# Kernel optimization log

Hardware: AMD Instinct MI355X
Metric: run time of the kernel (lower is better)

## Reference

```python
import jax, jax.numpy as jnp
import numpy as np

N_ENTITIES = 500000
N_RELATIONS = 16
DIM = 64
N_HOP = 2
BATCH = 256
N_MEMORY = 32


def setup_inputs() -> dict:
    key = jax.random.key(0)
    k1, k2, k3, k4, k5, k6 = jax.random.split(key, 6)
    entity_emb = jax.random.normal(k1, (N_ENTITIES + 1, DIM), dtype=jnp.float32) * 0.02
    relation_emb = jax.random.normal(k2, (N_RELATIONS, DIM), dtype=jnp.float32) * 0.02
    items = jax.random.randint(k3, (BATCH,), 0, N_ENTITIES)
    shape = (N_HOP, BATCH, N_RELATIONS, N_MEMORY)
    memories_h = jax.random.randint(k4, shape, 0, N_ENTITIES)
    memories_r = jax.random.randint(k5, shape, 0, N_RELATIONS)
    memories_t = jax.random.randint(k6, shape, 0, N_ENTITIES)
    return {
        "entity_emb": entity_emb,
        "relation_emb": relation_emb,
        "items": items,
        "memories_h": memories_h,
        "memories_r": memories_r,
        "memories_t": memories_t,
    }


def reference(entity_emb, relation_emb, items, memories_h, memories_r, memories_t):
    # items_emb / v: [B, D]
    v = entity_emb[items]

    def per_hop(mh, mr, mt):
        # gathers: [B, R, M, D]
        h = entity_emb[mh]
        r = relation_emb[mr]
        t = entity_emb[mt]
        # relation-modulated head: Rh = r * h  -> [B, R, M, D]
        Rh = r * h
        # attention scores against item embedding v: [B, R, M]
        scores = jnp.einsum("brmd,bd->brm", Rh, v)
        probs = jax.nn.softmax(scores, axis=-1)
        # weighted sum of tail embeddings: [B, R, D]
        return jnp.einsum("brmd,brm->brd", t, probs)

    # vmap over hop axis -> o: [n_hop, B, R, D]
    o = jax.vmap(per_hop)(memories_h, memories_r, memories_t)
    return o
```

## Files before the change

kernel.cpp:

```cpp
#include <hip/hip_runtime.h>
#include <hip/hip_bf16.h>

constexpr int BATCH = 256;
constexpr int NREL  = 16;
constexpr int DIM   = 64;
constexpr int NHOP  = 2;
constexpr int NMEM  = 32;

__global__ __launch_bounds__(256)
void kgan_kernel(const float* __restrict__ ent,
                 const float* __restrict__ rel,
                 const int*   __restrict__ items,
                 const int*   __restrict__ mh,
                 const int*   __restrict__ mr,
                 const int*   __restrict__ mt,
                 float*       __restrict__ out)
{
    __shared__ float rel_lds[NREL * DIM];
    {
        const int t = threadIdx.x;
        reinterpret_cast<float4*>(rel_lds)[t] =
            reinterpret_cast<const float4*>(rel)[t];
    }
    __syncthreads();

    const int gtid = blockIdx.x * blockDim.x + threadIdx.x;
    const int wave = gtid >> 6;
    const int lane = threadIdx.x & 63;
    const int sub  = lane >> 4;
    const int q    = lane & 15;

    const int b = (wave >> 4) & (BATCH - 1);

    const int item = items[b];
    const float4 v4 = reinterpret_cast<const float4*>(ent)[(size_t)item * 16 + q];

    const int base = wave * NMEM;
    const int lm   = lane & 31;
    const int vh   = mh[base + lm];
    const int vr   = mr[base + lm];
    const int vt   = mt[base + lm];

    const float4* ent4 = reinterpret_cast<const float4*>(ent);
    const float4* rl4  = reinterpret_cast<const float4*>(rel_lds);

    float4 hb[8], tb[8];
    int ridx[8];
    #pragma unroll
    for (int j = 0; j < 8; ++j) {
        const int hid = __shfl(vh, 4 * j + sub, 64);
        hb[j] = ent4[(size_t)hid * 16 + q];
    }
    #pragma unroll
    for (int j = 0; j < 8; ++j) {
        const int tid = __shfl(vt, 4 * j + sub, 64);
        tb[j] = ent4[(size_t)tid * 16 + q];
    }
    #pragma unroll
    for (int j = 0; j < 8; ++j)
        ridx[j] = __shfl(vr, 4 * j + sub, 64);

    float sc[8];
    #pragma unroll
    for (int j = 0; j < 8; ++j) {
        const float4 r4 = rl4[ridx[j] * 16 + q];
        const float4 h4 = hb[j];
        float p = h4.x * r4.x * v4.x;
        p = fmaf(h4.y * r4.y, v4.y, p);
        p = fmaf(h4.z * r4.z, v4.z, p);
        p = fmaf(h4.w * r4.w, v4.w, p);
        #pragma unroll
        for (int off = 8; off >= 1; off >>= 1)
            p += __shfl_xor(p, off, 64);
        sc[j] = p;
    }

    float mx = sc[0];
    #pragma unroll
    for (int j = 1; j < 8; ++j) mx = fmaxf(mx, sc[j]);
    mx = fmaxf(mx, __shfl_xor(mx, 16, 64));
    mx = fmaxf(mx, __shfl_xor(mx, 32, 64));

    float sum = 0.f;
    #pragma unroll
    for (int j = 0; j < 8; ++j) {
        sc[j] = __expf(sc[j] - mx);
        sum += sc[j];
    }
    sum += __shfl_xor(sum, 16, 64);
    sum += __shfl_xor(sum, 32, 64);
    const float inv = 1.f / sum;

    float4 acc = make_float4(0.f, 0.f, 0.f, 0.f);
    #pragma unroll
    for (int j = 0; j < 8; ++j) {
        const float p = sc[j] * inv;
        acc.x = fmaf(p, tb[j].x, acc.x);
        acc.y = fmaf(p, tb[j].y, acc.y);
        acc.z = fmaf(p, tb[j].z, acc.z);
        acc.w = fmaf(p, tb[j].w, acc.w);
    }
    acc.x += __shfl_xor(acc.x, 16, 64);
    acc.y += __shfl_xor(acc.y, 16, 64);
    acc.z += __shfl_xor(acc.z, 16, 64);
    acc.w += __shfl_xor(acc.w, 16, 64);
    acc.x += __shfl_xor(acc.x, 32, 64);
    acc.y += __shfl_xor(acc.y, 32, 64);
    acc.z += __shfl_xor(acc.z, 32, 64);
    acc.w += __shfl_xor(acc.w, 32, 64);

    if (sub == 0)
        reinterpret_cast<float4*>(out)[(size_t)wave * 16 + q] = acc;
}

extern "C" void kernel_launch(void* const* d_in, const int* in_sizes, int n_in,
                              void* d_out, int out_size, void* d_ws, size_t ws_size,
                              hipStream_t stream) {
    const float* ent   = (const float*)d_in[0];
    const float* rel   = (const float*)d_in[1];
    const int*   items = (const int*)d_in[2];
    const int*   mh    = (const int*)d_in[3];
    const int*   mr    = (const int*)d_in[4];
    const int*   mt    = (const int*)d_in[5];
    float* out = (float*)d_out;

    const int total_waves = NHOP * BATCH * NREL;
    const int threads = 256;
    const int blocks = total_waves * 64 / threads;

    kgan_kernel<<<blocks, threads, 0, stream>>>(ent, rel, items, mh, mr, mt, out);
}
```

Before: 25.35 us.

## Load memory indices as scalars and reuse head registers for tail gathers

Makes the wave index wave-uniform so the memory index arrays can be read as uniform (scalar) loads, and each lane picks its index with selects instead of cross-lane shuffles. Head embeddings are gathered first, and tail gathers are issued into the same registers once the matching scores are computed. This lowers vector register use and drops the shuffle work. The cost is more scalar loads and select instructions, and the tail gathers now depend on score computation finishing first, which can delay their issue.

```diff
diff --git a/kernel.cpp b/kernel.cpp
--- a/kernel.cpp
+++ b/kernel.cpp
@@ -6,6 +6,12 @@
 constexpr int DIM   = 64;
 constexpr int NHOP  = 2;
 constexpr int NMEM  = 32;
+
+__device__ __forceinline__ int pick4(int s0, int s1, int s2, int s3, int sub) {
+    const int ab = (sub & 1) ? s1 : s0;
+    const int cd = (sub & 1) ? s3 : s2;
+    return (sub & 2) ? cd : ab;
+}
 
 __global__ __launch_bounds__(256)
 void kgan_kernel(const float* __restrict__ ent,
@@ -17,63 +23,89 @@
                  float*       __restrict__ out)
 {
     __shared__ float rel_lds[NREL * DIM];
-    {
-        const int t = threadIdx.x;
-        reinterpret_cast<float4*>(rel_lds)[t] =
-            reinterpret_cast<const float4*>(rel)[t];
-    }
+    reinterpret_cast<float4*>(rel_lds)[threadIdx.x] =
+        reinterpret_cast<const float4*>(rel)[threadIdx.x];
     __syncthreads();
 
     const int gtid = blockIdx.x * blockDim.x + threadIdx.x;
-    const int wave = gtid >> 6;
     const int lane = threadIdx.x & 63;
     const int sub  = lane >> 4;
     const int q    = lane & 15;
-
-    const int b = (wave >> 4) & (BATCH - 1);
-
-    const int item = items[b];
-    const float4 v4 = reinterpret_cast<const float4*>(ent)[(size_t)item * 16 + q];
-
-    const int base = wave * NMEM;
-    const int lm   = lane & 31;
-    const int vh   = mh[base + lm];
-    const int vr   = mr[base + lm];
-    const int vt   = mt[base + lm];
+    const int wave = __builtin_amdgcn_readfirstlane(gtid >> 6);
+    const int b    = (wave >> 4) & (BATCH - 1);
 
     const float4* ent4 = reinterpret_cast<const float4*>(ent);
     const float4* rl4  = reinterpret_cast<const float4*>(rel_lds);
 
-    float4 hb[8], tb[8];
-    int ridx[8];
+    const int item = items[b];
+    const float4 v4 = ent4[(size_t)item * 16 + q];
+
+    const int* mhw = mh + wave * NMEM;
+    const int* mrw = mr + wave * NMEM;
+    const int* mtw = mt + wave * NMEM;
+
+    int sh[NMEM];
     #pragma unroll
-    for (int j = 0; j < 8; ++j) {
-        const int hid = __shfl(vh, 4 * j + sub, 64);
-        hb[j] = ent4[(size_t)hid * 16 + q];
-    }
+    for (int k = 0; k < NMEM; ++k) sh[k] = mhw[k];
+
+    auto gp = [&](int i0, int i1, int i2, int i3) -> const float4* {
+        const int idx = pick4(i0, i1, i2, i3, sub);
+        return ent4 + ((size_t)idx * 16 + q);
+    };
+
+    float4 A0 = *gp(sh[0],  sh[1],  sh[2],  sh[3]);
+    float4 A1 = *gp(sh[4],  sh[5],  sh[6],  sh[7]);
+    float4 A2 = *gp(sh[8],  sh[9],  sh[10], sh[11]);
+    float4 A3 = *gp(sh[12], sh[13], sh[14], sh[15]);
+    float4 B0 = *gp(sh[16], sh[17], sh[18], sh[19]);
+    float4 B1 = *gp(sh[20], sh[21], sh[22], sh[23]);
+    float4 B2 = *gp(sh[24], sh[25], sh[26], sh[27]);
+    float4 B3 = *gp(sh[28], sh[29], sh[30], sh[31]);
+
+    int sr[NMEM];
     #pragma unroll
-    for (int j = 0; j < 8; ++j) {
-        const int tid = __shfl(vt, 4 * j + sub, 64);
-        tb[j] = ent4[(size_t)tid * 16 + q];
-    }
-    #pragma unroll
-    for (int j = 0; j < 8; ++j)
-        ridx[j] = __shfl(vr, 4 * j + sub, 64);
+    for (int k = 0; k < NMEM; ++k) sr[k] = mrw[k];
 
     float sc[8];
-    #pragma unroll
-    for (int j = 0; j < 8; ++j) {
-        const float4 r4 = rl4[ridx[j] * 16 + q];
-        const float4 h4 = hb[j];
+    auto score = [&](const float4& h4, int j) -> float {
+        const int rj = pick4(sr[4*j], sr[4*j+1], sr[4*j+2], sr[4*j+3], sub);
+        const float4 r4 = rl4[rj * 16 + q];
         float p = h4.x * r4.x * v4.x;
         p = fmaf(h4.y * r4.y, v4.y, p);
         p = fmaf(h4.z * r4.z, v4.z, p);
         p = fmaf(h4.w * r4.w, v4.w, p);
-        #pragma unroll
-        for (int off = 8; off >= 1; off >>= 1)
-            p += __shfl_xor(p, off, 64);
-        sc[j] = p;
-    }
+        p += __shfl_xor(p, 8, 64);
+        p += __shfl_xor(p, 4, 64);
+        p += __shfl_xor(p, 2, 64);
+        p += __shfl_xor(p, 1, 64);
+        return p;
+    };
+
+    sc[0] = score(A0, 0);
+    sc[1] = score(A1, 1);
+    sc[2] = score(A2, 2);
+    sc[3] = score(A3, 3);
+
+    int st0[16];
+    #pragma unroll
+    for (int k = 0; k < 16; ++k) st0[k] = mtw[k];
+    A0 = *gp(st0[0],  st0[1],  st0[2],  st0[3]);
+    A1 = *gp(st0[4],  st0[5],  st0[6],  st0[7]);
+    A2 = *gp(st0[8],  st0[9],  st0[10], st0[11]);
+    A3 = *gp(st0[12], st0[13], st0[14], st0[15]);
+
+    sc[4] = score(B0, 4);
+    sc[5] = score(B1, 5);
+    sc[6] = score(B2, 6);
+    sc[7] = score(B3, 7);
+
+    int st1[16];
+    #pragma unroll
+    for (int k = 0; k < 16; ++k) st1[k] = mtw[16 + k];
+    B0 = *gp(st1[0],  st1[1],  st1[2],  st1[3]);
+    B1 = *gp(st1[4],  st1[5],  st1[6],  st1[7]);
+    B2 = *gp(st1[8],  st1[9],  st1[10], st1[11]);
+    B3 = *gp(st1[12], st1[13], st1[14], st1[15]);
 
     float mx = sc[0];
     #pragma unroll
@@ -92,14 +124,21 @@
     const float inv = 1.f / sum;
 
     float4 acc = make_float4(0.f, 0.f, 0.f, 0.f);
-    #pragma unroll
-    for (int j = 0; j < 8; ++j) {
-        const float p = sc[j] * inv;
-        acc.x = fmaf(p, tb[j].x, acc.x);
-        acc.y = fmaf(p, tb[j].y, acc.y);
-        acc.z = fmaf(p, tb[j].z, acc.z);
-        acc.w = fmaf(p, tb[j].w, acc.w);
-    }
+    auto pv = [&](const float4& t4, float p) {
+        acc.x = fmaf(p, t4.x, acc.x);
+        acc.y = fmaf(p, t4.y, acc.y);
+        acc.z = fmaf(p, t4.z, acc.z);
+        acc.w = fmaf(p, t4.w, acc.w);
+    };
+    pv(A0, sc[0] * inv);
+    pv(A1, sc[1] * inv);
+    pv(A2, sc[2] * inv);
+    pv(A3, sc[3] * inv);
+    pv(B0, sc[4] * inv);
+    pv(B1, sc[5] * inv);
+    pv(B2, sc[6] * inv);
+    pv(B3, sc[7] * inv);
+
     acc.x += __shfl_xor(acc.x, 16, 64);
     acc.y += __shfl_xor(acc.y, 16, 64);
     acc.z += __shfl_xor(acc.z, 16, 64);
```

New measurement: 26.35 us. 3.9% more time.

## Split each memory row across two waves with LDS softmax merge

Applied to the files above, without the earlier changes.

Each (hop,batch,relation) row is now handled by two waves, each gathering 16 of the 32 memory slots. The per-wave softmax max and sum are exchanged through shared memory and combined online, and the partial weighted sums are added through an LDS buffer before one wave writes the result. This doubles the wave count and halves the per-wave gather depth to expose more memory parallelism for the random entity gathers. In exchange it adds two block barriers, LDS traffic, and redundant loads of the item embedding and relation table.

```diff
diff --git a/kernel.cpp b/kernel.cpp
--- a/kernel.cpp
+++ b/kernel.cpp
@@ -16,85 +16,96 @@
                  const int*   __restrict__ mt,
                  float*       __restrict__ out)
 {
-    __shared__ float rel_lds[NREL * DIM];
-    {
-        const int t = threadIdx.x;
-        reinterpret_cast<float4*>(rel_lds)[t] =
-            reinterpret_cast<const float4*>(rel)[t];
-    }
+    __shared__ float  rel_lds[NREL * DIM];
+    __shared__ float  stats[4][2];
+    __shared__ float4 pvbuf[4][16];
+
+    reinterpret_cast<float4*>(rel_lds)[threadIdx.x] =
+        reinterpret_cast<const float4*>(rel)[threadIdx.x];
     __syncthreads();
 
-    const int gtid = blockIdx.x * blockDim.x + threadIdx.x;
-    const int wave = gtid >> 6;
-    const int lane = threadIdx.x & 63;
-    const int sub  = lane >> 4;
-    const int q    = lane & 15;
+    const int gtid   = blockIdx.x * blockDim.x + threadIdx.x;
+    const int lane   = threadIdx.x & 63;
+    const int wgwave = threadIdx.x >> 6;
+    const int wave   = gtid >> 6;
+    const int trip   = wave >> 1;
+    const int hf     = wave & 1;
+    const int sub    = lane >> 4;
+    const int q      = lane & 15;
 
-    const int b = (wave >> 4) & (BATCH - 1);
+    const int b = (trip >> 4) & (BATCH - 1);
+
+    const float4* ent4 = reinterpret_cast<const float4*>(ent);
+    const float4* rl4  = reinterpret_cast<const float4*>(rel_lds);
 
     const int item = items[b];
-    const float4 v4 = reinterpret_cast<const float4*>(ent)[(size_t)item * 16 + q];
+    const float4 v4 = ent4[(size_t)item * 16 + q];
 
-    const int base = wave * NMEM;
-    const int lm   = lane & 31;
+    const int base = trip * NMEM + hf * 16;
+    const int lm   = lane & 15;
     const int vh   = mh[base + lm];
     const int vr   = mr[base + lm];
     const int vt   = mt[base + lm];
 
-    const float4* ent4 = reinterpret_cast<const float4*>(ent);
-    const float4* rl4  = reinterpret_cast<const float4*>(rel_lds);
-
-    float4 hb[8], tb[8];
-    int ridx[8];
+    float4 hb[4], tb[4];
+    int ridx[4];
     #pragma unroll
-    for (int j = 0; j < 8; ++j) {
+    for (int j = 0; j < 4; ++j) {
         const int hid = __shfl(vh, 4 * j + sub, 64);
         hb[j] = ent4[(size_t)hid * 16 + q];
     }
     #pragma unroll
-    for (int j = 0; j < 8; ++j) {
+    for (int j = 0; j < 4; ++j) {
         const int tid = __shfl(vt, 4 * j + sub, 64);
         tb[j] = ent4[(size_t)tid * 16 + q];
     }
     #pragma unroll
-    for (int j = 0; j < 8; ++j)
+    for (int j = 0; j < 4; ++j)
         ridx[j] = __shfl(vr, 4 * j + sub, 64);
 
-    float sc[8];
+    float sc[4];
     #pragma unroll
-    for (int j = 0; j < 8; ++j) {
+    for (int j = 0; j < 4; ++j) {
         const float4 r4 = rl4[ridx[j] * 16 + q];
         const float4 h4 = hb[j];
         float p = h4.x * r4.x * v4.x;
         p = fmaf(h4.y * r4.y, v4.y, p);
         p = fmaf(h4.z * r4.z, v4.z, p);
         p = fmaf(h4.w * r4.w, v4.w, p);
-        #pragma unroll
-        for (int off = 8; off >= 1; off >>= 1)
-            p += __shfl_xor(p, off, 64);
+        p += __shfl_xor(p, 8, 64);
+        p += __shfl_xor(p, 4, 64);
+        p += __shfl_xor(p, 2, 64);
+        p += __shfl_xor(p, 1, 64);
         sc[j] = p;
     }
 
-    float mx = sc[0];
-    #pragma unroll
-    for (int j = 1; j < 8; ++j) mx = fmaxf(mx, sc[j]);
+    float mx = fmaxf(fmaxf(sc[0], sc[1]), fmaxf(sc[2], sc[3]));
     mx = fmaxf(mx, __shfl_xor(mx, 16, 64));
     mx = fmaxf(mx, __shfl_xor(mx, 32, 64));
 
     float sum = 0.f;
     #pragma unroll
-    for (int j = 0; j < 8; ++j) {
+    for (int j = 0; j < 4; ++j) {
         sc[j] = __expf(sc[j] - mx);
         sum += sc[j];
     }
     sum += __shfl_xor(sum, 16, 64);
     sum += __shfl_xor(sum, 32, 64);
-    const float inv = 1.f / sum;
+
+    if (lane == 0) { stats[wgwave][0] = mx; stats[wgwave][1] = sum; }
+    __syncthreads();
+
+    const int prt = wgwave ^ 1;
+    const float m1 = stats[prt][0], s1 = stats[prt][1];
+    const float ms = fmaxf(mx, m1);
+    const float f0 = __expf(mx - ms);
+    const float tot = sum * f0 + s1 * __expf(m1 - ms);
+    const float scale = f0 / tot;
 
     float4 acc = make_float4(0.f, 0.f, 0.f, 0.f);
     #pragma unroll
-    for (int j = 0; j < 8; ++j) {
-        const float p = sc[j] * inv;
+    for (int j = 0; j < 4; ++j) {
+        const float p = sc[j] * scale;
         acc.x = fmaf(p, tb[j].x, acc.x);
         acc.y = fmaf(p, tb[j].y, acc.y);
         acc.z = fmaf(p, tb[j].z, acc.z);
@@ -109,8 +120,14 @@
     acc.z += __shfl_xor(acc.z, 32, 64);
     acc.w += __shfl_xor(acc.w, 32, 64);
 
-    if (sub == 0)
-        reinterpret_cast<float4*>(out)[(size_t)wave * 16 + q] = acc;
+    if (sub == 0) pvbuf[wgwave][q] = acc;
+    __syncthreads();
+
+    if (hf == 0 && sub == 0) {
+        const float4 p2 = pvbuf[wgwave + 1][q];
+        acc.x += p2.x; acc.y += p2.y; acc.z += p2.z; acc.w += p2.w;
+        reinterpret_cast<float4*>(out)[(size_t)trip * 16 + q] = acc;
+    }
 }
 
 extern "C" void kernel_launch(void* const* d_in, const int* in_sizes, int n_in,
@@ -124,7 +141,7 @@
     const int*   mt    = (const int*)d_in[5];
     float* out = (float*)d_out;
 
-    const int total_waves = NHOP * BATCH * NREL;
+    const int total_waves = NHOP * BATCH * NREL * 2;
     const int threads = 256;
     const int blocks = total_waves * 64 / threads;
 
```

Measured after the change: 26.01 us. 2.6% more time.
